# Kernel optimization log

Measured on AMD Instinct MI355X. Metric: run time of the kernel, lower is better.

## Reference

```python
import jax, jax.numpy as jnp
import numpy as np

N = 50000
E = 625000
D_IN, D_HID, D_OUT = 128, 128, 64


def setup_inputs() -> dict:
    key = jax.random.key(0)
    k1, k2, k3, k4 = jax.random.split(key, 4)
    x = jax.random.normal(k1, (N, D_IN), dtype=jnp.float32)
    edge_index = jax.random.randint(k2, (2, E), 0, N, dtype=jnp.int32)
    # Glorot-ish init for linear weights (PyG lin has no bias; bias added after agg)
    W1 = jax.random.normal(k3, (D_HID, D_IN), dtype=jnp.float32) / np.sqrt(D_IN)
    b1 = jnp.zeros((D_HID,), dtype=jnp.float32)
    W2 = jax.random.normal(k4, (D_OUT, D_HID), dtype=jnp.float32) / np.sqrt(D_HID)
    b2 = jnp.zeros((D_OUT,), dtype=jnp.float32)
    return {"x": x, "edge_index": edge_index, "W1": W1, "b1": b1, "W2": W2, "b2": b2}


def _gcn_conv(x, W, b, src, dst, n):
    # GCNConv: h = x @ W^T; out[dst] += norm * h[src]; out += b
    # src/dst already include self-loops; symmetric normalization deg^{-1/2}.
    ones = jnp.ones(src.shape[0], dtype=x.dtype)
    deg = jax.ops.segment_sum(ones, dst, num_segments=n)
    dinv = jnp.where(deg > 0, jax.lax.rsqrt(deg), 0.0)
    norm = dinv[src] * dinv[dst]                      # [E+N]
    h = x @ W.T                                        # [N, d_out]
    msg = norm[:, None] * h[src]                       # [E+N, d_out]
    out = jax.ops.segment_sum(msg, dst, num_segments=n)
    return out + b


def reference(x, edge_index, W1, b1, W2, b2):
    n = x.shape[0]
    loops = jnp.arange(n, dtype=edge_index.dtype)
    src = jnp.concatenate([edge_index[0], loops])      # add self-loops
    dst = jnp.concatenate([edge_index[1], loops])
    h = _gcn_conv(x, W1, b1, src, dst, n)
    h = jax.nn.relu(h)
    out = _gcn_conv(h, W2, b2, src, dst, n)
    return out
```

## Files before the change

kernel.cpp:

```cpp
#include <hip/hip_runtime.h>
#include <hip/hip_bf16.h>


typedef __attribute__((ext_vector_type(8))) __bf16 bf16x8;
typedef __attribute__((ext_vector_type(8))) unsigned short ushort8;
typedef __attribute__((ext_vector_type(4))) float floatx4;

static __device__ __forceinline__ float bf2f(unsigned short s) {
    unsigned u = ((unsigned)s) << 16;
    return __builtin_bit_cast(float, u);
}
static __device__ __forceinline__ unsigned short f2bf(float f) {
    unsigned u = __builtin_bit_cast(unsigned, f);
    unsigned r = (u + 0x7FFFu + ((u >> 16) & 1u)) >> 16;
    return (unsigned short)r;
}
static __device__ __forceinline__ void ld8f(const void* p, size_t idx, int isbf, float* o) {
    if (isbf) {
        ushort8 t = __builtin_bit_cast(ushort8, *(const int4*)((const unsigned short*)p + idx));
        #pragma unroll
        for (int j = 0; j < 8; ++j) o[j] = bf2f(t[j]);
    } else {
        const float* f = (const float*)p + idx;
        float4 a = *(const float4*)f;
        float4 b = *(const float4*)(f + 4);
        o[0]=a.x; o[1]=a.y; o[2]=a.z; o[3]=a.w; o[4]=b.x; o[5]=b.y; o[6]=b.z; o[7]=b.w;
    }
}
static __device__ __forceinline__ int4 ld8frag(const void* p, size_t idx, int isbf) {
    if (isbf) {
        return *(const int4*)((const unsigned short*)p + idx);
    } else {
        const float* f = (const float*)p + idx;
        float4 a = *(const float4*)f;
        float4 b = *(const float4*)(f + 4);
        ushort8 t;
        t[0]=f2bf(a.x); t[1]=f2bf(a.y); t[2]=f2bf(a.z); t[3]=f2bf(a.w);
        t[4]=f2bf(b.x); t[5]=f2bf(b.y); t[6]=f2bf(b.z); t[7]=f2bf(b.w);
        return __builtin_bit_cast(int4, t);
    }
}
static __device__ __forceinline__ float bread(const void* p, int i, int isbf) {
    return isbf ? bf2f(((const unsigned short*)p)[i]) : ((const float*)p)[i];
}

__global__ __launch_bounds__(256) void k_countdet(
    const int* __restrict__ dst, int* __restrict__ cnt, int E, int EB,
    const unsigned* __restrict__ xw, int* __restrict__ flag)
{
    int b = blockIdx.x;
    if (b == EB) {
        __shared__ int red[256];
        int t = threadIdx.x;
        int c = 0;
        #pragma unroll
        for (int i = 0; i < 16; ++i) {
            unsigned w = xw[t * 16 + i];
            unsigned exp = (w >> 7) & 0xFFu;
            c += (exp <= 0x84u) ? 1 : 0;
        }
        red[t] = c;
        __syncthreads();
        for (int s = 128; s > 0; s >>= 1) {
            if (t < s) red[t] += red[t + s];
            __syncthreads();
        }
        if (t == 0) flag[0] = (red[0] >= 3686) ? 1 : 0;
        return;
    }
    int e = b * 256 + threadIdx.x;
    if (e < E) atomicAdd(&cnt[dst[e]], 1);
}

__global__ __launch_bounds__(256) void k_scanA(
    const int* __restrict__ cnt, int* __restrict__ partial, int N)
{
    int b = blockIdx.x, t = threadIdx.x;
    int base = b * 1024 + t * 4;
    int s = 0;
    if (base + 3 < N) {
        int4 v = *(const int4*)&cnt[base];
        s = v.x + v.y + v.z + v.w;
    } else {
        for (int j = 0; j < 4; ++j) { int i = base + j; if (i < N) s += cnt[i]; }
    }
    #pragma unroll
    for (int d = 1; d < 64; d <<= 1) s += __shfl_down(s, d, 64);
    __shared__ int ws[4];
    int lane = t & 63, wid = t >> 6;
    if (lane == 0) ws[wid] = s;
    __syncthreads();
    if (t == 0) partial[b] = ws[0] + ws[1] + ws[2] + ws[3];
}

__global__ __launch_bounds__(256) void k_scanC(
    const int* __restrict__ cnt, const int* __restrict__ partial,
    int* __restrict__ off, int* __restrict__ cursor, float* __restrict__ dinv,
    int N, int nb)
{
    __shared__ int s_pref, s_tot;
    int b = blockIdx.x, t = threadIdx.x, lane = t & 63, wid = t >> 6;
    if (t == 0) {
        int s = 0, pb = 0;
        for (int i = 0; i < nb; ++i) { if (i == b) pb = s; s += partial[i]; }
        s_pref = pb; s_tot = s;
    }
    int base = b * 1024 + t * 4;
    int v[4], s = 0;
    #pragma unroll
    for (int j = 0; j < 4; ++j) {
        int i = base + j;
        v[j] = (i < N) ? cnt[i] : 0;
        s += v[j];
    }
    int x = s;
    #pragma unroll
    for (int d = 1; d < 64; d <<= 1) {
        int u = __shfl_up(x, d, 64);
        if (lane >= d) x += u;
    }
    __shared__ int wtot[4], woff[4];
    if (lane == 63) wtot[wid] = x;
    __syncthreads();
    if (t == 0) {
        int a = 0;
        #pragma unroll
        for (int w = 0; w < 4; ++w) { woff[w] = a; a += wtot[w]; }
    }
    __syncthreads();
    int excl = s_pref + woff[wid] + (x - s);
    #pragma unroll
    for (int j = 0; j < 4; ++j) {
        int i = base + j;
        if (i < N) {
            off[i] = excl;
            cursor[i] = excl;
            dinv[i] = rsqrtf(1.0f + (float)v[j]);
            excl += v[j];
        }
    }
    if (b == 0 && t == 0) off[N] = s_tot;
}

__global__ void k_scatter(const int* __restrict__ src, const int* __restrict__ dst,
                          int* __restrict__ cursor, int* __restrict__ bucket, int E) {
    int e = blockIdx.x * 256 + threadIdx.x;
    if (e >= E) return;
    int pos = atomicAdd(&cursor[dst[e]], 1);
    bucket[pos] = src[e];
}

__global__ __launch_bounds__(256) void k_gather1(
    const void* __restrict__ x, const float* __restrict__ dinv,
    const int* __restrict__ off, const int* __restrict__ bucket,
    float* __restrict__ buf, int N, const int* __restrict__ flag)
{
    int isbf = *flag;
    int gid = blockIdx.x * 256 + threadIdx.x;
    int node = gid >> 4, p = gid & 15;
    if (node >= N) return;
    float di = dinv[node];
    float acc[8], va[8], vb[8];
    ld8f(x, (size_t)node * 128 + p * 8, isbf, va);
    float w0 = di * di;
    #pragma unroll
    for (int j = 0; j < 8; ++j) acc[j] = w0 * va[j];
    int it = off[node], s1 = off[node + 1];
    for (; it + 1 < s1; it += 2) {
        int sa = bucket[it], sb = bucket[it + 1];
        float wa = di * dinv[sa], wb = di * dinv[sb];
        ld8f(x, (size_t)sa * 128 + p * 8, isbf, va);
        ld8f(x, (size_t)sb * 128 + p * 8, isbf, vb);
        #pragma unroll
        for (int j = 0; j < 8; ++j) acc[j] += wa * va[j] + wb * vb[j];
    }
    if (it < s1) {
        int sa = bucket[it];
        float wa = di * dinv[sa];
        ld8f(x, (size_t)sa * 128 + p * 8, isbf, va);
        #pragma unroll
        for (int j = 0; j < 8; ++j) acc[j] += wa * va[j];
    }
    float* o = &buf[(size_t)node * 128 + p * 8];
    float4 a = {acc[0], acc[1], acc[2], acc[3]};
    float4 b = {acc[4], acc[5], acc[6], acc[7]};
    *(float4*)o = a;
    *(float4*)(o + 4) = b;
}

__global__ __launch_bounds__(256) void k_gemm12(
    float* buf, const void* __restrict__ W1, const void* __restrict__ b1,
    const void* __restrict__ W2, int N, const int* __restrict__ flag)
{
    int isbf = *flag;
    __shared__ int4 w1f[2048];
    __shared__ unsigned short h1t[4][16 * 136];
    int tid = threadIdx.x;
    for (int u = tid; u < 2048; u += 256) {
        int nt = u >> 8, kt = (u >> 6) & 3, lane = u & 63;
        int so = (nt * 16 + (lane & 15)) * 128 + kt * 32 + ((lane >> 4) << 3);
        w1f[u] = ld8frag(W1, so, isbf);
    }
    int wave = tid >> 6, lane = tid & 63, m = lane & 15, quad = lane >> 4;

    int4 w2r[4][4];
    #pragma unroll
    for (int nt = 0; nt < 4; ++nt)
        #pragma unroll
        for (int kt = 0; kt < 4; ++kt)
            w2r[nt][kt] = ld8frag(W2, (nt * 16 + m) * 128 + kt * 32 + quad * 8, isbf);
    __syncthreads();

    int ntile = (N + 15) >> 4;
    int tile = blockIdx.x * 4 + wave;
    int tcl = (tile < ntile) ? tile : (ntile - 1);
    int arow = tcl * 16 + m;
    if (arow >= N) arow = N - 1;

    bf16x8 a[4];
    #pragma unroll
    for (int kt = 0; kt < 4; ++kt) {
        const float* p = &buf[(size_t)arow * 128 + kt * 32 + quad * 8];
        float4 f0 = *(const float4*)p;
        float4 f1 = *(const float4*)(p + 4);
        ushort8 t;
        t[0]=f2bf(f0.x); t[1]=f2bf(f0.y); t[2]=f2bf(f0.z); t[3]=f2bf(f0.w);
        t[4]=f2bf(f1.x); t[5]=f2bf(f1.y); t[6]=f2bf(f1.z); t[7]=f2bf(f1.w);
        a[kt] = __builtin_bit_cast(bf16x8, t);
    }
    floatx4 acc[8];
    floatx4 z = {0.f, 0.f, 0.f, 0.f};
    #pragma unroll
    for (int nt = 0; nt < 8; ++nt) acc[nt] = z;
    #pragma unroll
    for (int kt = 0; kt < 4; ++kt)
        #pragma unroll
        for (int nt = 0; nt < 8; ++nt) {
            bf16x8 b = __builtin_bit_cast(bf16x8, w1f[nt * 256 + kt * 64 + lane]);
            acc[nt] = __builtin_amdgcn_mfma_f32_16x16x32_bf16(a[kt], b, acc[nt], 0, 0, 0);
        }
    #pragma unroll
    for (int nt = 0; nt < 8; ++nt) {
        int col = nt * 16 + m;
        float bb = bread(b1, col, isbf);
        #pragma unroll
        for (int r = 0; r < 4; ++r) {
            float v = acc[nt][r] + bb;
            h1t[wave][(quad * 4 + r) * 136 + col] = f2bf(fmaxf(v, 0.f));
        }
    }
    __syncthreads();

    bf16x8 a2[4];
    #pragma unroll
    for (int kt = 0; kt < 4; ++kt)
        a2[kt] = __builtin_bit_cast(bf16x8, *(const int4*)&h1t[wave][m * 136 + kt * 32 + quad * 8]);
    floatx4 acc2[4];
    #pragma unroll
    for (int nt = 0; nt < 4; ++nt) acc2[nt] = z;
    #pragma unroll
    for (int kt = 0; kt < 4; ++kt)
        #pragma unroll
        for (int nt = 0; nt < 4; ++nt) {
            bf16x8 b = __builtin_bit_cast(bf16x8, w2r[nt][kt]);
            acc2[nt] = __builtin_amdgcn_mfma_f32_16x16x32_bf16(a2[kt], b, acc2[nt], 0, 0, 0);
        }
    if (tile < ntile) {
        unsigned short* h2 = (unsigned short*)buf;
        int rbase = tcl * 16 + quad * 4;
        #pragma unroll
        for (int nt = 0; nt < 4; ++nt) {
            int col = nt * 16 + m;
            #pragma unroll
            for (int r = 0; r < 4; ++r) {
                int orow = rbase + r;
                if (orow < N)
                    h2[(size_t)orow * 256 + col] = f2bf(acc2[nt][r]);
            }
        }
    }
}

__global__ __launch_bounds__(256) void k_gather2(
    const float* __restrict__ buf, const float* __restrict__ dinv,
    const int* __restrict__ off, const int* __restrict__ bucket,
    const void* __restrict__ b2, void* __restrict__ out, int N,
    const int* __restrict__ flag)
{
    int isbf = *flag;
    int gid = blockIdx.x * 256 + threadIdx.x;
    int node = gid >> 3, p = gid & 7;
    if (node >= N) return;
    const unsigned short* h2 = (const unsigned short*)buf;
    float di = dinv[node];
    float acc[8];
    {
        ushort8 t = __builtin_bit_cast(ushort8, *(const int4*)&h2[(size_t)node * 256 + p * 8]);
        float w0 = di * di;
        #pragma unroll
        for (int j = 0; j < 8; ++j) acc[j] = w0 * bf2f(t[j]);
    }
    int it = off[node], s1 = off[node + 1];
    for (; it + 1 < s1; it += 2) {
        int sa = bucket[it], sb = bucket[it + 1];
        float wa = di * dinv[sa], wb = di * dinv[sb];
        ushort8 ta = __builtin_bit_cast(ushort8, *(const int4*)&h2[(size_t)sa * 256 + p * 8]);
        ushort8 tb = __builtin_bit_cast(ushort8, *(const int4*)&h2[(size_t)sb * 256 + p * 8]);
        #pragma unroll
        for (int j = 0; j < 8; ++j) acc[j] += wa * bf2f(ta[j]) + wb * bf2f(tb[j]);
    }
    if (it < s1) {
        int sa = bucket[it];
        float wa = di * dinv[sa];
        ushort8 ta = __builtin_bit_cast(ushort8, *(const int4*)&h2[(size_t)sa * 256 + p * 8]);
        #pragma unroll
        for (int j = 0; j < 8; ++j) acc[j] += wa * bf2f(ta[j]);
    }
    #pragma unroll
    for (int j = 0; j < 8; ++j) acc[j] += bread(b2, p * 8 + j, isbf);
    if (isbf) {
        ushort8 o;
        #pragma unroll
        for (int j = 0; j < 8; ++j) o[j] = f2bf(acc[j]);
        *(int4*)((unsigned short*)out + (size_t)node * 64 + p * 8) = __builtin_bit_cast(int4, o);
    } else {
        float* fo = (float*)out + (size_t)node * 64 + p * 8;
        float4 a = {acc[0], acc[1], acc[2], acc[3]};
        float4 b = {acc[4], acc[5], acc[6], acc[7]};
        *(float4*)fo = a;
        *(float4*)(fo + 4) = b;
    }
}

extern "C" void kernel_launch(void* const* d_in, const int* in_sizes, int n_in,
                              void* d_out, int out_size, void* d_ws, size_t ws_size,
                              hipStream_t stream) {
    const void* x  = d_in[0];
    const int*  ei = (const int*)d_in[1];
    const void* W1 = d_in[2];
    const void* b1 = d_in[3];
    const void* W2 = d_in[4];
    const void* b2 = d_in[5];

    int N = in_sizes[0] / 128;
    int E = in_sizes[1] / 2;
    const int* srcI = ei;
    const int* dstI = ei + E;

    int nb = (N + 1023) / 1024;
    int EB = (E + 255) / 256;

    char* base = (char*)d_ws;
    size_t o = 0;
    auto take = [&](size_t bytes) { size_t r = o; o += (bytes + 255) & ~(size_t)255; return r; };
    int*   flag    = (int*)  (base + take(4));
    int*   cnt     = (int*)  (base + take((size_t)N * 4));
    int*   off     = (int*)  (base + take((size_t)(N + 1) * 4));
    int*   cursor  = (int*)  (base + take((size_t)N * 4));
    float* dinv    = (float*)(base + take((size_t)N * 4));
    int*   partial = (int*)  (base + take((size_t)nb * 4));
    int*   bucket  = (int*)  (base + take((size_t)E * 4));
    float* buf     = (float*)(base + take((size_t)N * 512));

    int ntile = (N + 15) / 16;
    int gemmBlocks = (ntile + 3) / 4;

    hipMemsetAsync(cnt, 0, (size_t)N * 4, stream);
    k_countdet<<<EB + 1, 256, 0, stream>>>(dstI, cnt, E, EB, (const unsigned*)x, flag);
    k_scanA<<<nb, 256, 0, stream>>>(cnt, partial, N);
    k_scanC<<<nb, 256, 0, stream>>>(cnt, partial, off, cursor, dinv, N, nb);
    k_scatter<<<EB, 256, 0, stream>>>(srcI, dstI, cursor, bucket, E);
    k_gather1<<<(N * 16 + 255) / 256, 256, 0, stream>>>(x, dinv, off, bucket, buf, N, flag);
    k_gemm12<<<gemmBlocks, 256, 0, stream>>>(buf, W1, b1, W2, N, flag);
    k_gather2<<<(N * 8 + 255) / 256, 256, 0, stream>>>(buf, dinv, off, bucket, b2, d_out, N, flag);
}
```

Baseline: 246.8 us.

## Precompute edge weights in scatter and store intermediates compactly in bf16

The scatter kernel now writes (src, norm-weight) pairs, so both gather kernels no longer do a dependent random dinv[src] load per edge. Gather1 writes its aggregate as bf16 instead of fp32, and the GEMM reads it directly without converting. The h2 buffer is packed at a 64-column stride instead of 256, which makes each row's gathered data contiguous. In exchange the bucket array doubles in size, the scatter does extra loads, and the intermediate is rounded to bf16 earlier, though the GEMM already rounded it to bf16 before.

```diff
diff --git a/kernel.cpp b/kernel.cpp
--- a/kernel.cpp
+++ b/kernel.cpp
@@ -143,17 +143,21 @@
 }
 
 __global__ void k_scatter(const int* __restrict__ src, const int* __restrict__ dst,
-                          int* __restrict__ cursor, int* __restrict__ bucket, int E) {
+                          const float* __restrict__ dinv,
+                          int* __restrict__ cursor, int2* __restrict__ bucket, int E) {
     int e = blockIdx.x * 256 + threadIdx.x;
     if (e >= E) return;
-    int pos = atomicAdd(&cursor[dst[e]], 1);
-    bucket[pos] = src[e];
+    int s = src[e], d = dst[e];
+    float w = dinv[s] * dinv[d];
+    int pos = atomicAdd(&cursor[d], 1);
+    int2 rec; rec.x = s; rec.y = __builtin_bit_cast(int, w);
+    bucket[pos] = rec;
 }
 
 __global__ __launch_bounds__(256) void k_gather1(
     const void* __restrict__ x, const float* __restrict__ dinv,
-    const int* __restrict__ off, const int* __restrict__ bucket,
-    float* __restrict__ buf, int N, const int* __restrict__ flag)
+    const int* __restrict__ off, const int2* __restrict__ bucket,
+    unsigned short* __restrict__ z1, int N, const int* __restrict__ flag)
 {
     int isbf = *flag;
     int gid = blockIdx.x * 256 + threadIdx.x;
@@ -167,30 +171,31 @@
     for (int j = 0; j < 8; ++j) acc[j] = w0 * va[j];
     int it = off[node], s1 = off[node + 1];
     for (; it + 1 < s1; it += 2) {
-        int sa = bucket[it], sb = bucket[it + 1];
-        float wa = di * dinv[sa], wb = di * dinv[sb];
-        ld8f(x, (size_t)sa * 128 + p * 8, isbf, va);
-        ld8f(x, (size_t)sb * 128 + p * 8, isbf, vb);
+        int2 ea = bucket[it], eb = bucket[it + 1];
+        float wa = __builtin_bit_cast(float, ea.y);
+        float wb = __builtin_bit_cast(float, eb.y);
+        ld8f(x, (size_t)ea.x * 128 + p * 8, isbf, va);
+        ld8f(x, (size_t)eb.x * 128 + p * 8, isbf, vb);
         #pragma unroll
         for (int j = 0; j < 8; ++j) acc[j] += wa * va[j] + wb * vb[j];
     }
     if (it < s1) {
-        int sa = bucket[it];
-        float wa = di * dinv[sa];
-        ld8f(x, (size_t)sa * 128 + p * 8, isbf, va);
+        int2 ea = bucket[it];
+        float wa = __builtin_bit_cast(float, ea.y);
+        ld8f(x, (size_t)ea.x * 128 + p * 8, isbf, va);
         #pragma unroll
         for (int j = 0; j < 8; ++j) acc[j] += wa * va[j];
     }
-    float* o = &buf[(size_t)node * 128 + p * 8];
-    float4 a = {acc[0], acc[1], acc[2], acc[3]};
-    float4 b = {acc[4], acc[5], acc[6], acc[7]};
-    *(float4*)o = a;
-    *(float4*)(o + 4) = b;
+    ushort8 o;
+    #pragma unroll
+    for (int j = 0; j < 8; ++j) o[j] = f2bf(acc[j]);
+    *(int4*)&z1[(size_t)node * 128 + p * 8] = __builtin_bit_cast(int4, o);
 }
 
 __global__ __launch_bounds__(256) void k_gemm12(
-    float* buf, const void* __restrict__ W1, const void* __restrict__ b1,
-    const void* __restrict__ W2, int N, const int* __restrict__ flag)
+    const unsigned short* __restrict__ z1, const void* __restrict__ W1,
+    const void* __restrict__ b1, const void* __restrict__ W2,
+    unsigned short* __restrict__ h2, int N, const int* __restrict__ flag)
 {
     int isbf = *flag;
     __shared__ int4 w1f[2048];
@@ -219,15 +224,8 @@
 
     bf16x8 a[4];
     #pragma unroll
-    for (int kt = 0; kt < 4; ++kt) {
-        const float* p = &buf[(size_t)arow * 128 + kt * 32 + quad * 8];
-        float4 f0 = *(const float4*)p;
-        float4 f1 = *(const float4*)(p + 4);
-        ushort8 t;
-        t[0]=f2bf(f0.x); t[1]=f2bf(f0.y); t[2]=f2bf(f0.z); t[3]=f2bf(f0.w);
-        t[4]=f2bf(f1.x); t[5]=f2bf(f1.y); t[6]=f2bf(f1.z); t[7]=f2bf(f1.w);
-        a[kt] = __builtin_bit_cast(bf16x8, t);
-    }
+    for (int kt = 0; kt < 4; ++kt)
+        a[kt] = __builtin_bit_cast(bf16x8, *(const int4*)&z1[(size_t)arow * 128 + kt * 32 + quad * 8]);
     floatx4 acc[8];
     floatx4 z = {0.f, 0.f, 0.f, 0.f};
     #pragma unroll
@@ -266,7 +264,6 @@
             acc2[nt] = __builtin_amdgcn_mfma_f32_16x16x32_bf16(a2[kt], b, acc2[nt], 0, 0, 0);
         }
     if (tile < ntile) {
-        unsigned short* h2 = (unsigned short*)buf;
         int rbase = tcl * 16 + quad * 4;
         #pragma unroll
         for (int nt = 0; nt < 4; ++nt) {
@@ -275,15 +272,15 @@
             for (int r = 0; r < 4; ++r) {
                 int orow = rbase + r;
                 if (orow < N)
-                    h2[(size_t)orow * 256 + col] = f2bf(acc2[nt][r]);
+                    h2[(size_t)orow * 64 + col] = f2bf(acc2[nt][r]);
             }
         }
     }
 }
 
 __global__ __launch_bounds__(256) void k_gather2(
-    const float* __restrict__ buf, const float* __restrict__ dinv,
-    const int* __restrict__ off, const int* __restrict__ bucket,
+    const unsigned short* __restrict__ h2, const float* __restrict__ dinv,
+    const int* __restrict__ off, const int2* __restrict__ bucket,
     const void* __restrict__ b2, void* __restrict__ out, int N,
     const int* __restrict__ flag)
 {
@@ -291,28 +288,28 @@
     int gid = blockIdx.x * 256 + threadIdx.x;
     int node = gid >> 3, p = gid & 7;
     if (node >= N) return;
-    const unsigned short* h2 = (const unsigned short*)buf;
     float di = dinv[node];
     float acc[8];
     {
-        ushort8 t = __builtin_bit_cast(ushort8, *(const int4*)&h2[(size_t)node * 256 + p * 8]);
+        ushort8 t = __builtin_bit_cast(ushort8, *(const int4*)&h2[(size_t)node * 64 + p * 8]);
         float w0 = di * di;
         #pragma unroll
         for (int j = 0; j < 8; ++j) acc[j] = w0 * bf2f(t[j]);
     }
     int it = off[node], s1 = off[node + 1];
     for (; it + 1 < s1; it += 2) {
-        int sa = bucket[it], sb = bucket[it + 1];
-        float wa = di * dinv[sa], wb = di * dinv[sb];
-        ushort8 ta = __builtin_bit_cast(ushort8, *(const int4*)&h2[(size_t)sa * 256 + p * 8]);
-        ushort8 tb = __builtin_bit_cast(ushort8, *(const int4*)&h2[(size_t)sb * 256 + p * 8]);
+        int2 ea = bucket[it], eb = bucket[it + 1];
+        float wa = __builtin_bit_cast(float, ea.y);
+        float wb = __builtin_bit_cast(float, eb.y);
+        ushort8 ta = __builtin_bit_cast(ushort8, *(const int4*)&h2[(size_t)ea.x * 64 + p * 8]);
+        ushort8 tb = __builtin_bit_cast(ushort8, *(const int4*)&h2[(size_t)eb.x * 64 + p * 8]);
         #pragma unroll
         for (int j = 0; j < 8; ++j) acc[j] += wa * bf2f(ta[j]) + wb * bf2f(tb[j]);
     }
     if (it < s1) {
-        int sa = bucket[it];
-        float wa = di * dinv[sa];
-        ushort8 ta = __builtin_bit_cast(ushort8, *(const int4*)&h2[(size_t)sa * 256 + p * 8]);
+        int2 ea = bucket[it];
+        float wa = __builtin_bit_cast(float, ea.y);
+        ushort8 ta = __builtin_bit_cast(ushort8, *(const int4*)&h2[(size_t)ea.x * 64 + p * 8]);
         #pragma unroll
         for (int j = 0; j < 8; ++j) acc[j] += wa * bf2f(ta[j]);
     }
@@ -359,8 +356,9 @@
     int*   cursor  = (int*)  (base + take((size_t)N * 4));
     float* dinv    = (float*)(base + take((size_t)N * 4));
     int*   partial = (int*)  (base + take((size_t)nb * 4));
-    int*   bucket  = (int*)  (base + take((size_t)E * 4));
-    float* buf     = (float*)(base + take((size_t)N * 512));
+    int2*  bucket  = (int2*) (base + take((size_t)E * 8));
+    unsigned short* z1 = (unsigned short*)(base + take((size_t)N * 128 * 2));
+    unsigned short* h2 = (unsigned short*)(base + take((size_t)N * 64 * 2));
 
     int ntile = (N + 15) / 16;
     int gemmBlocks = (ntile + 3) / 4;
@@ -369,8 +367,8 @@
     k_countdet<<<EB + 1, 256, 0, stream>>>(dstI, cnt, E, EB, (const unsigned*)x, flag);
     k_scanA<<<nb, 256, 0, stream>>>(cnt, partial, N);
     k_scanC<<<nb, 256, 0, stream>>>(cnt, partial, off, cursor, dinv, N, nb);
-    k_scatter<<<EB, 256, 0, stream>>>(srcI, dstI, cursor, bucket, E);
-    k_gather1<<<(N * 16 + 255) / 256, 256, 0, stream>>>(x, dinv, off, bucket, buf, N, flag);
-    k_gemm12<<<gemmBlocks, 256, 0, stream>>>(buf, W1, b1, W2, N, flag);
-    k_gather2<<<(N * 8 + 255) / 256, 256, 0, stream>>>(buf, dinv, off, bucket, b2, d_out, N, flag);
-}
+    k_scatter<<<EB, 256, 0, stream>>>(srcI, dstI, dinv, cursor, bucket, E);
+    k_gather1<<<(N * 16 + 255) / 256, 256, 0, stream>>>(x, dinv, off, bucket, z1, N, flag);
+    k_gemm12<<<gemmBlocks, 256, 0, stream>>>(z1, W1, b1, W2, h2, N, flag);
+    k_gather2<<<(N * 8 + 255) / 256, 256, 0, stream>>>(h2, dinv, off, bucket, b2, d_out, N, flag);
+}
```

Result: no change. 250.5 us (+1.5%).
